# Kernel optimization log

Hardware: AMD Instinct MI355X
Metric: run time of the kernel (lower is better)

## Reference

```python
import jax, jax.numpy as jnp
import numpy as np

GAMMA = 0.99
ALPHA = 0.01
EPS = 1e-08


def discounted_returns(rewards, gamma):
    # reverse linear recurrence G_t = r_t + gamma * G_{t+1}, scanned over time (dim 0)
    def step(G, r):
        G = r + gamma * G
        return G, G
    G0 = jnp.zeros(rewards.shape[1:], dtype=rewards.dtype)
    _, returns = jax.lax.scan(step, G0, rewards, reverse=True)
    return returns


def setup_inputs() -> dict:
    key = jax.random.key(0)
    k1, k2, k3, k4, k5 = jax.random.split(key, 5)
    T, B = 8192, 4096
    return {
        "rewards": jax.random.normal(k1, (T, B), dtype=jnp.float32),
        "value_estimates": jax.random.normal(k2, (T, B), dtype=jnp.float32),
        "log_probs": jax.random.normal(k3, (T, B), dtype=jnp.float32),
        "entropies": jax.random.uniform(k4, (T, B), dtype=jnp.float32),
        "to_include": jax.random.randint(k5, (T, B), 0, 2) > 0,
    }


def reference(rewards, value_estimates, log_probs, entropies, to_include):
    returns = discounted_returns(rewards, GAMMA)

    mask = to_include.astype(returns.dtype)
    n = jnp.sum(mask)
    # first call: count=1 -> sg=0 -> running stats equal masked batch stats (detached)
    mean = jax.lax.stop_gradient(jnp.sum(returns * mask) / n)
    var = jnp.sum(jnp.square((returns - mean) * mask)) / (n - 1.0)  # torch .std() is unbiased
    std = jax.lax.stop_gradient(jnp.sqrt(var))

    returns = (returns - mean) / (std + EPS)
    advantages = returns - value_estimates

    critic_loss = jnp.sum(jnp.square(advantages) * mask)
    actor_terms = -log_probs * jax.lax.stop_gradient(advantages) - ALPHA * entropies
    actor_loss = jnp.sum(actor_terms * mask)
    return (critic_loss, actor_loss)
```

## Files before the change

kernel.cpp:

```cpp
#include <hip/hip_runtime.h>
#include <hip/hip_cooperative_groups.h>

namespace cg = cooperative_groups;


constexpr int T     = 8192;
constexpr int B     = 4096;
constexpr int B4    = B / 4;
constexpr int BLK   = 256;
constexpr int WAVES = BLK / 64;
constexpr int L     = 32;
constexpr int NC    = T / L;
constexpr int NTILE = NC * 4;
constexpr int GSZ   = 16;
constexpr int NGRP  = NC / GSZ;

constexpr float GAMMA_F = 0.99f;
constexpr double cpow(double g, int n) { double r = 1.0; for (int i = 0; i < n; ++i) r *= g; return r; }
constexpr float G32  = (float)cpow(0.99, L);
constexpr float G512 = (float)cpow(0.99, L * GSZ);

#define COMP(MJ, GX, RX, VX, LX, ZX)                 \
    do {                                             \
        GX = fmaf(GAMMA_F, GX, RX);                  \
        float mm = (MJ);                             \
        float Gm = mm * GX, vm = mm * VX, lm = mm * LX; \
        a[0] += mm; a[1] += Gm;                      \
        a[2] = fmaf(Gm, GX, a[2]);                   \
        a[3] = fmaf(Gm, VX, a[3]);                   \
        a[4] += vm; a[5] = fmaf(vm, VX, a[5]);       \
        a[6] = fmaf(lm, GX, a[6]); a[7] += lm;       \
        a[8] = fmaf(mm, ZX, a[8]);                   \
        a[9] = fmaf(lm, VX, a[9]);                   \
    } while (0)

#define MASK_I32 { int4 q = ((const int4*)mp)[e]; \
    m0 = q.x ? 1.f : 0.f; m1 = q.y ? 1.f : 0.f; m2 = q.z ? 1.f : 0.f; m3 = q.w ? 1.f : 0.f; }
#define MASK_U8  { uchar4 q = ((const uchar4*)mp)[e]; \
    m0 = q.x ? 1.f : 0.f; m1 = q.y ? 1.f : 0.f; m2 = q.z ? 1.f : 0.f; m3 = q.w ? 1.f : 0.f; }

#define ITER_BODY(MASKLOAD)                          \
    _Pragma("unroll 4")                              \
    for (int i = L - 1; i >= 0; --i) {               \
        int e = base + i * B4;                       \
        float4 r = rw[e], v = vv[e], l = lq[e], z = en[e]; \
        float m0, m1, m2, m3;                        \
        MASKLOAD;                                    \
        COMP(m0, G.x, r.x, v.x, l.x, z.x);           \
        COMP(m1, G.y, r.y, v.y, l.y, z.y);           \
        COMP(m2, G.z, r.z, v.z, l.z, z.z);           \
        COMP(m3, G.w, r.w, v.w, l.w, z.w);           \
    }

__device__ __forceinline__ float4 chunk_scan(const float4* __restrict__ rw, int base) {
    const float g2 = GAMMA_F * GAMMA_F;
    float4 e4 = make_float4(0.f, 0.f, 0.f, 0.f);
    float4 o4 = make_float4(0.f, 0.f, 0.f, 0.f);
    #pragma unroll
    for (int j = L / 2 - 1; j >= 0; --j) {
        float4 ro = rw[base + (2 * j + 1) * B4];
        float4 re = rw[base + (2 * j) * B4];
        o4.x = fmaf(g2, o4.x, ro.x); o4.y = fmaf(g2, o4.y, ro.y);
        o4.z = fmaf(g2, o4.z, ro.z); o4.w = fmaf(g2, o4.w, ro.w);
        e4.x = fmaf(g2, e4.x, re.x); e4.y = fmaf(g2, e4.y, re.y);
        e4.z = fmaf(g2, e4.z, re.z); e4.w = fmaf(g2, e4.w, re.w);
    }
    float4 s;
    s.x = fmaf(GAMMA_F, o4.x, e4.x); s.y = fmaf(GAMMA_F, o4.y, e4.y);
    s.z = fmaf(GAMMA_F, o4.z, e4.z); s.w = fmaf(GAMMA_F, o4.w, e4.w);
    return s;
}

__device__ __forceinline__ float4 chunk_carry(const float4* __restrict__ S,
                                              const float4* __restrict__ Hg,
                                              int c, int b) {
    const int g = c >> 4;
    const int gend = (g << 4) | (GSZ - 1);
    float4 X = make_float4(0.f, 0.f, 0.f, 0.f);
    float w = 1.f;
    for (int cc = c + 1; cc <= gend; ++cc) {
        float4 sv = S[(size_t)cc * B4 + b];
        X.x = fmaf(w, sv.x, X.x); X.y = fmaf(w, sv.y, X.y);
        X.z = fmaf(w, sv.z, X.z); X.w = fmaf(w, sv.w, X.w);
        w *= G32;
    }
    float4 hg = Hg[(size_t)g * B4 + b];
    X.x = fmaf(w, hg.x, X.x); X.y = fmaf(w, hg.y, X.y);
    X.z = fmaf(w, hg.z, X.z); X.w = fmaf(w, hg.w, X.w);
    return X;
}

__device__ __forceinline__ void fold_groups(const float4* __restrict__ S,
                                            float4* __restrict__ Sg,
                                            int idx) {
    int g = idx >> 10;
    int bb = idx & 1023;
    float4 X = make_float4(0.f, 0.f, 0.f, 0.f);
    float w = 1.f;
    #pragma unroll
    for (int j = 0; j < GSZ; ++j) {
        float4 sv = S[(size_t)(g * GSZ + j) * B4 + bb];
        X.x = fmaf(w, sv.x, X.x); X.y = fmaf(w, sv.y, X.y);
        X.z = fmaf(w, sv.z, X.z); X.w = fmaf(w, sv.w, X.w);
        w *= G32;
    }
    Sg[(size_t)g * B4 + bb] = X;
}

__device__ __forceinline__ void gscan_col(const float4* __restrict__ Sg,
                                          float4* __restrict__ Hg, int bb) {
    float4 h = make_float4(0.f, 0.f, 0.f, 0.f);
    #pragma unroll
    for (int g = NGRP - 1; g >= 0; --g) {
        Hg[(size_t)g * B4 + bb] = h;
        float4 sv = Sg[(size_t)g * B4 + bb];
        h.x = fmaf(G512, h.x, sv.x); h.y = fmaf(G512, h.y, sv.y);
        h.z = fmaf(G512, h.z, sv.z); h.w = fmaf(G512, h.w, sv.w);
    }
}

__device__ __forceinline__ void finalize(const double s[10], float* out) {
    double n = s[0], SG = s[1], SG2 = s[2], SGv = s[3], Sv = s[4];
    double Sv2 = s[5], SlpG = s[6], Slp = s[7], Sent = s[8], Slpv = s[9];
    double mean = SG / n;
    double css  = SG2 - 2.0 * mean * SG + mean * mean * n;
    double var  = css / (n - 1.0);
    double sd   = sqrt(var);
    double sc   = 1.0 / (sd + 1e-8);
    double critic = sc * sc * css - 2.0 * sc * (SGv - mean * Sv) + Sv2;
    double actor  = -sc * (SlpG - mean * Slp) + Slpv - 0.01 * Sent;
    out[0] = (float)critic;
    out[1] = (float)actor;
}

__device__ __forceinline__ void reduce10_store(double d[10], double* dst,
                                               double shd[WAVES][10], int tid) {
    #pragma unroll
    for (int k = 0; k < 10; ++k)
        #pragma unroll
        for (int off = 32; off; off >>= 1)
            d[k] += __shfl_down(d[k], off);
    int lane = tid & 63, wv = tid >> 6;
    if (lane == 0) {
        #pragma unroll
        for (int k = 0; k < 10; ++k) shd[wv][k] = d[k];
    }
    __syncthreads();
    if (tid == 0) {
        #pragma unroll
        for (int k = 0; k < 10; ++k) {
            double t = shd[0][k];
            #pragma unroll
            for (int ww = 1; ww < WAVES; ++ww) t += shd[ww][k];
            dst[k] = t;
        }
    }
}

__device__ __forceinline__ void final_reduce(const double* __restrict__ p1,
                                             double shd[WAVES][10],
                                             int tid, float* out) {
    double d[10];
    #pragma unroll
    for (int k = 0; k < 10; ++k) d[k] = 0.0;
    for (int i = tid; i < NTILE; i += BLK) {
        #pragma unroll
        for (int k = 0; k < 10; ++k) d[k] += p1[(size_t)i * 10 + k];
    }
    #pragma unroll
    for (int k = 0; k < 10; ++k)
        #pragma unroll
        for (int off = 32; off; off >>= 1)
            d[k] += __shfl_down(d[k], off);
    int lane = tid & 63, wv = tid >> 6;
    if (lane == 0) {
        #pragma unroll
        for (int k = 0; k < 10; ++k) shd[wv][k] = d[k];
    }
    __syncthreads();
    if (tid == 0) {
        double s[10];
        #pragma unroll
        for (int k = 0; k < 10; ++k) {
            double t = shd[0][k];
            #pragma unroll
            for (int ww = 1; ww < WAVES; ++ww) t += shd[ww][k];
            s[k] = t;
        }
        finalize(s, out);
    }
}

__global__ void __launch_bounds__(BLK, 4) k_all(
    const float4* __restrict__ rw, const float4* __restrict__ vv,
    const float4* __restrict__ lq, const float4* __restrict__ en,
    const void*  __restrict__ mp,
    float4* __restrict__ S, float4* __restrict__ Sg, float4* __restrict__ Hg,
    double* __restrict__ p1, float* __restrict__ out)
{
    cg::grid_group grid = cg::this_grid();
    const int tid = threadIdx.x;
    const int bid = blockIdx.x;
    const int c = bid >> 2, s = bid & 3;
    const int b = s * 256 + tid;
    const int base = c * L * B4 + b;

    __shared__ double shd[WAVES][10];
    __shared__ unsigned shp[WAVES];

    unsigned pv = 0;
    {
        const uint4* mq = (const uint4*)mp;
        #pragma unroll
        for (int it = 0; it < 4; ++it) {
            uint4 q = mq[it * BLK + tid];
            pv |= (q.x | q.y | q.z | q.w) & 0xFFFFFF00u;
        }
        #pragma unroll
        for (int off = 32; off; off >>= 1) pv |= __shfl_down(pv, off);
        if ((tid & 63) == 0) shp[tid >> 6] = pv;
        __syncthreads();
        pv = shp[0] | shp[1] | shp[2] | shp[3];
    }
    const bool is32 = (pv == 0);

    S[(size_t)c * B4 + b] = chunk_scan(rw, base);
    grid.sync();

    if (bid < NGRP * B4 / BLK) fold_groups(S, Sg, bid * BLK + tid);
    grid.sync();

    if (bid < B4 / BLK) gscan_col(Sg, Hg, bid * BLK + tid);
    grid.sync();

    {
        float4 G = chunk_carry(S, Hg, c, b);
        float a[10] = {0.f, 0.f, 0.f, 0.f, 0.f, 0.f, 0.f, 0.f, 0.f, 0.f};
        if (is32) { ITER_BODY(MASK_I32); }
        else      { ITER_BODY(MASK_U8); }
        double d[10];
        #pragma unroll
        for (int k = 0; k < 10; ++k) d[k] = (double)a[k];
        reduce10_store(d, p1 + (size_t)bid * 10, shd, tid);
    }
    grid.sync();

    if (bid == 0) final_reduce(p1, shd, tid, out);
}

__global__ void __launch_bounds__(BLK) k_scanf(const float4* __restrict__ rw,
                                               const void* __restrict__ mp,
                                               float4* __restrict__ S,
                                               int* __restrict__ dflag) {
    __shared__ unsigned shp[WAVES];
    const int tid = threadIdx.x, bid = blockIdx.x;
    const int c = bid >> 2, s = bid & 3;
    const int b = s * 256 + tid;
    S[(size_t)c * B4 + b] = chunk_scan(rw, c * L * B4 + b);
    if (bid == NTILE - 1) {
        unsigned pv = 0;
        const uint4* mq = (const uint4*)mp;
        #pragma unroll
        for (int it = 0; it < 4; ++it) {
            uint4 q = mq[it * BLK + tid];
            pv |= (q.x | q.y | q.z | q.w) & 0xFFFFFF00u;
        }
        #pragma unroll
        for (int off = 32; off; off >>= 1) pv |= __shfl_down(pv, off);
        if ((tid & 63) == 0) shp[tid >> 6] = pv;
        __syncthreads();
        if (tid == 0) *dflag = ((shp[0] | shp[1] | shp[2] | shp[3]) == 0) ? 1 : 0;
    }
}

__global__ void __launch_bounds__(BLK) k_foldf(const float4* __restrict__ S,
                                               float4* __restrict__ Sg) {
    fold_groups(S, Sg, blockIdx.x * BLK + threadIdx.x);
}

__global__ void __launch_bounds__(BLK) k_gscanf(const float4* __restrict__ Sg,
                                                float4* __restrict__ Hg) {
    gscan_col(Sg, Hg, blockIdx.x * BLK + threadIdx.x);
}

__global__ void __launch_bounds__(BLK) k_mainf(const float4* __restrict__ rw,
                                               const float4* __restrict__ vv,
                                               const float4* __restrict__ lq,
                                               const float4* __restrict__ en,
                                               const void*  __restrict__ mp,
                                               const int*   __restrict__ dflag,
                                               const float4* __restrict__ S,
                                               const float4* __restrict__ Hg,
                                               double* __restrict__ p1) {
    __shared__ double shd[WAVES][10];
    const int tid = threadIdx.x, bid = blockIdx.x;
    const int c = bid >> 2, s = bid & 3;
    const int b = s * 256 + tid;
    const int base = c * L * B4 + b;
    float4 G = chunk_carry(S, Hg, c, b);
    float a[10] = {0.f, 0.f, 0.f, 0.f, 0.f, 0.f, 0.f, 0.f, 0.f, 0.f};
    if (*dflag) { ITER_BODY(MASK_I32); }
    else        { ITER_BODY(MASK_U8); }
    double d[10];
    #pragma unroll
    for (int k = 0; k < 10; ++k) d[k] = (double)a[k];
    reduce10_store(d, p1 + (size_t)bid * 10, shd, tid);
}

__global__ void __launch_bounds__(BLK) k_finalf(const double* __restrict__ p1,
                                                float* __restrict__ out) {
    __shared__ double shd[WAVES][10];
    final_reduce(p1, shd, threadIdx.x, out);
}

extern "C" void kernel_launch(void* const* d_in, const int* in_sizes, int n_in,
                              void* d_out, int out_size, void* d_ws, size_t ws_size,
                              hipStream_t stream) {
    const float4* rw = (const float4*)d_in[0];
    const float4* vv = (const float4*)d_in[1];
    const float4* lq = (const float4*)d_in[2];
    const float4* en = (const float4*)d_in[3];
    const void*   mp = d_in[4];

    char* ws = (char*)d_ws;
    size_t off = 0;
    float4* S   = (float4*)(ws + off); off += (size_t)NC * B4 * 16;
    float4* Sg  = (float4*)(ws + off); off += (size_t)NGRP * B4 * 16;
    float4* Hg  = (float4*)(ws + off); off += (size_t)NGRP * B4 * 16;
    double* p1  = (double*)(ws + off); off += (size_t)NTILE * 10 * 8;
    int*  dflag = (int*)  (ws + off);
    float* outp = (float*)d_out;

    int dev = 0;
    (void)hipGetDevice(&dev);
    int coop = 0, ncu = 0, maxb = 0;
    (void)hipDeviceGetAttribute(&coop, hipDeviceAttributeCooperativeLaunch, dev);
    (void)hipDeviceGetAttribute(&ncu, hipDeviceAttributeMultiprocessorCount, dev);
    bool use_coop = false;
    if (coop) {
        if (hipOccupancyMaxActiveBlocksPerMultiprocessor(&maxb, k_all, BLK, 0)
                == hipSuccess && (long)maxb * ncu >= NTILE)
            use_coop = true;
    }
    if (use_coop) {
        void* args[] = { (void*)&rw, (void*)&vv, (void*)&lq, (void*)&en,
                         (void*)&mp, (void*)&S, (void*)&Sg, (void*)&Hg,
                         (void*)&p1, (void*)&outp };
        if (hipLaunchCooperativeKernel((void*)k_all, dim3(NTILE), dim3(BLK),
                                       args, 0, stream) != hipSuccess)
            use_coop = false;
    }
    if (!use_coop) {
        k_scanf <<<NTILE, BLK, 0, stream>>>(rw, mp, S, dflag);
        k_foldf <<<NGRP * B4 / BLK, BLK, 0, stream>>>(S, Sg);
        k_gscanf<<<B4 / BLK, BLK, 0, stream>>>(Sg, Hg);
        k_mainf <<<NTILE, BLK, 0, stream>>>(rw, vv, lq, en, mp, dflag, S, Hg, p1);
        k_finalf<<<1, BLK, 0, stream>>>(p1, outp);
    }
}
```

Before: 152.0 us.

## Single-pass input read with carry-correction coefficients instead of second sweep

```diff
diff --git a/kernel.cpp b/kernel.cpp
--- a/kernel.cpp
+++ b/kernel.cpp
@@ -14,11 +14,48 @@
 constexpr int NTILE = NC * 4;
 constexpr int GSZ   = 16;
 constexpr int NGRP  = NC / GSZ;
+constexpr int NTHR  = NTILE * BLK;
 
 constexpr float GAMMA_F = 0.99f;
 constexpr double cpow(double g, int n) { double r = 1.0; for (int i = 0; i < n; ++i) r *= g; return r; }
 constexpr float G32  = (float)cpow(0.99, L);
 constexpr float G512 = (float)cpow(0.99, L * GSZ);
+
+#define COMPC(MJ, GX, RX, VX, LX, ZX, C0X, C1X, C2X, C3X, C4X)   \
+    do {                                                         \
+        GX = fmaf(GAMMA_F, GX, RX);                              \
+        float mm = (MJ);                                         \
+        float Gm = mm * GX, vm = mm * VX, lm = mm * LX, mw = mm * w; \
+        a[0] += mm; a[1] += Gm;                                  \
+        a[2] = fmaf(Gm, GX, a[2]); a[3] = fmaf(Gm, VX, a[3]);    \
+        a[4] += vm; a[5] = fmaf(vm, VX, a[5]);                   \
+        a[6] = fmaf(lm, GX, a[6]); a[7] += lm;                   \
+        a[8] = fmaf(mm, ZX, a[8]); a[9] = fmaf(lm, VX, a[9]);    \
+        C0X += mw;                                               \
+        C1X = fmaf(mw, GX, C1X);                                 \
+        C2X = fmaf(mw, w,  C2X);                                 \
+        C3X = fmaf(mw, VX, C3X);                                 \
+        C4X = fmaf(mw, LX, C4X);                                 \
+    } while (0)
+
+#define MASK_I32 { int4 q = ((const int4*)mp)[e]; \
+    m0 = q.x ? 1.f : 0.f; m1 = q.y ? 1.f : 0.f; m2 = q.z ? 1.f : 0.f; m3 = q.w ? 1.f : 0.f; }
+#define MASK_U8  { uchar4 q = ((const uchar4*)mp)[e]; \
+    m0 = q.x ? 1.f : 0.f; m1 = q.y ? 1.f : 0.f; m2 = q.z ? 1.f : 0.f; m3 = q.w ? 1.f : 0.f; }
+
+#define ITER_BODYC(MASKLOAD)                         \
+    _Pragma("unroll 4")                              \
+    for (int i = L - 1; i >= 0; --i) {               \
+        int e = base + i * B4;                       \
+        float4 r = rw[e], v = vv[e], l = lq[e], z = en[e]; \
+        float m0, m1, m2, m3;                        \
+        MASKLOAD;                                    \
+        COMPC(m0, G.x, r.x, v.x, l.x, z.x, c0.x, c1.x, c2.x, c3.x, c4.x); \
+        COMPC(m1, G.y, r.y, v.y, l.y, z.y, c0.y, c1.y, c2.y, c3.y, c4.y); \
+        COMPC(m2, G.z, r.z, v.z, l.z, z.z, c0.z, c1.z, c2.z, c3.z, c4.z); \
+        COMPC(m3, G.w, r.w, v.w, l.w, z.w, c0.w, c1.w, c2.w, c3.w, c4.w); \
+        w *= GAMMA_F;                                \
+    }
 
 #define COMP(MJ, GX, RX, VX, LX, ZX)                 \
     do {                                             \
@@ -34,11 +71,6 @@
         a[9] = fmaf(lm, VX, a[9]);                   \
     } while (0)
 
-#define MASK_I32 { int4 q = ((const int4*)mp)[e]; \
-    m0 = q.x ? 1.f : 0.f; m1 = q.y ? 1.f : 0.f; m2 = q.z ? 1.f : 0.f; m3 = q.w ? 1.f : 0.f; }
-#define MASK_U8  { uchar4 q = ((const uchar4*)mp)[e]; \
-    m0 = q.x ? 1.f : 0.f; m1 = q.y ? 1.f : 0.f; m2 = q.z ? 1.f : 0.f; m3 = q.w ? 1.f : 0.f; }
-
 #define ITER_BODY(MASKLOAD)                          \
     _Pragma("unroll 4")                              \
     for (int i = L - 1; i >= 0; --i) {               \
@@ -91,8 +123,7 @@
 }
 
 __device__ __forceinline__ void fold_groups(const float4* __restrict__ S,
-                                            float4* __restrict__ Sg,
-                                            int idx) {
+                                            float4* __restrict__ Sg, int idx) {
     int g = idx >> 10;
     int bb = idx & 1023;
     float4 X = make_float4(0.f, 0.f, 0.f, 0.f);
@@ -157,37 +188,27 @@
     }
 }
 
-__device__ __forceinline__ void final_reduce(const double* __restrict__ p1,
-                                             double shd[WAVES][10],
-                                             int tid, float* out) {
-    double d[10];
-    #pragma unroll
-    for (int k = 0; k < 10; ++k) d[k] = 0.0;
-    for (int i = tid; i < NTILE; i += BLK) {
-        #pragma unroll
-        for (int k = 0; k < 10; ++k) d[k] += p1[(size_t)i * 10 + k];
-    }
-    #pragma unroll
-    for (int k = 0; k < 10; ++k)
+__device__ __forceinline__ void reduce4_store(double d[4], double* dst,
+                                              double shd[WAVES][10], int tid) {
+    #pragma unroll
+    for (int k = 0; k < 4; ++k)
         #pragma unroll
         for (int off = 32; off; off >>= 1)
             d[k] += __shfl_down(d[k], off);
     int lane = tid & 63, wv = tid >> 6;
     if (lane == 0) {
         #pragma unroll
-        for (int k = 0; k < 10; ++k) shd[wv][k] = d[k];
+        for (int k = 0; k < 4; ++k) shd[wv][k] = d[k];
     }
     __syncthreads();
     if (tid == 0) {
-        double s[10];
-        #pragma unroll
-        for (int k = 0; k < 10; ++k) {
+        #pragma unroll
+        for (int k = 0; k < 4; ++k) {
             double t = shd[0][k];
             #pragma unroll
             for (int ww = 1; ww < WAVES; ++ww) t += shd[ww][k];
-            s[k] = t;
-        }
-        finalize(s, out);
+            dst[k] = t;
+        }
     }
 }
 
@@ -196,7 +217,9 @@
     const float4* __restrict__ lq, const float4* __restrict__ en,
     const void*  __restrict__ mp,
     float4* __restrict__ S, float4* __restrict__ Sg, float4* __restrict__ Hg,
-    double* __restrict__ p1, float* __restrict__ out)
+    float4* __restrict__ CF0, float4* __restrict__ CF1, float4* __restrict__ CF2,
+    float4* __restrict__ CF3, float4* __restrict__ CF4,
+    double* __restrict__ p1, double* __restrict__ p2, float* __restrict__ out)
 {
     cg::grid_group grid = cg::this_grid();
     const int tid = threadIdx.x;
@@ -204,6 +227,7 @@
     const int c = bid >> 2, s = bid & 3;
     const int b = s * 256 + tid;
     const int base = c * L * B4 + b;
+    const size_t gt = (size_t)bid * BLK + tid;
 
     __shared__ double shd[WAVES][10];
     __shared__ unsigned shp[WAVES];
@@ -224,7 +248,22 @@
     }
     const bool is32 = (pv == 0);
 
-    S[(size_t)c * B4 + b] = chunk_scan(rw, base);
+    {
+        float4 G  = make_float4(0.f, 0.f, 0.f, 0.f);
+        float4 c0 = G, c1 = G, c2 = G, c3 = G, c4 = G;
+        float a[10] = {0.f, 0.f, 0.f, 0.f, 0.f, 0.f, 0.f, 0.f, 0.f, 0.f};
+        float w = GAMMA_F;
+        if (is32) { ITER_BODYC(MASK_I32); }
+        else      { ITER_BODYC(MASK_U8); }
+
+        S[(size_t)c * B4 + b] = G;
+        CF0[gt] = c0; CF1[gt] = c1; CF2[gt] = c2; CF3[gt] = c3; CF4[gt] = c4;
+
+        double d[10];
+        #pragma unroll
+        for (int k = 0; k < 10; ++k) d[k] = (double)a[k];
+        reduce10_store(d, p1 + (size_t)bid * 10, shd, tid);
+    }
     grid.sync();
 
     if (bid < NGRP * B4 / BLK) fold_groups(S, Sg, bid * BLK + tid);
@@ -234,18 +273,54 @@
     grid.sync();
 
     {
-        float4 G = chunk_carry(S, Hg, c, b);
-        float a[10] = {0.f, 0.f, 0.f, 0.f, 0.f, 0.f, 0.f, 0.f, 0.f, 0.f};
-        if (is32) { ITER_BODY(MASK_I32); }
-        else      { ITER_BODY(MASK_U8); }
+        float4 X = chunk_carry(S, Hg, c, b);
+        float4 c0 = CF0[gt], c1 = CF1[gt], c2 = CF2[gt], c3 = CF3[gt], c4 = CF4[gt];
+        double hx = X.x, hy = X.y, hz = X.z, hw = X.w;
+        double d[4];
+        d[0] = hx * c0.x + hy * c0.y + hz * c0.z + hw * c0.w;
+        d[1] = 2.0 * (hx * c1.x + hy * c1.y + hz * c1.z + hw * c1.w)
+             + (hx * hx * c2.x + hy * hy * c2.y + hz * hz * c2.z + hw * hw * c2.w);
+        d[2] = hx * c3.x + hy * c3.y + hz * c3.z + hw * c3.w;
+        d[3] = hx * c4.x + hy * c4.y + hz * c4.z + hw * c4.w;
+        reduce4_store(d, p2 + (size_t)bid * 4, shd, tid);
+    }
+    grid.sync();
+
+    if (bid == 0) {
         double d[10];
         #pragma unroll
-        for (int k = 0; k < 10; ++k) d[k] = (double)a[k];
-        reduce10_store(d, p1 + (size_t)bid * 10, shd, tid);
-    }
-    grid.sync();
-
-    if (bid == 0) final_reduce(p1, shd, tid, out);
+        for (int k = 0; k < 10; ++k) d[k] = 0.0;
+        for (int i = tid; i < NTILE; i += BLK) {
+            #pragma unroll
+            for (int k = 0; k < 10; ++k) d[k] += p1[(size_t)i * 10 + k];
+            d[1] += p2[(size_t)i * 4 + 0];
+            d[2] += p2[(size_t)i * 4 + 1];
+            d[3] += p2[(size_t)i * 4 + 2];
+            d[6] += p2[(size_t)i * 4 + 3];
+        }
+        #pragma unroll
+        for (int k = 0; k < 10; ++k)
+            #pragma unroll
+            for (int off = 32; off; off >>= 1)
+                d[k] += __shfl_down(d[k], off);
+        int lane = tid & 63, wv = tid >> 6;
+        if (lane == 0) {
+            #pragma unroll
+            for (int k = 0; k < 10; ++k) shd[wv][k] = d[k];
+        }
+        __syncthreads();
+        if (tid == 0) {
+            double sum[10];
+            #pragma unroll
+            for (int k = 0; k < 10; ++k) {
+                double t = shd[0][k];
+                #pragma unroll
+                for (int ww = 1; ww < WAVES; ++ww) t += shd[ww][k];
+                sum[k] = t;
+            }
+            finalize(sum, out);
+        }
+    }
 }
 
 __global__ void __launch_bounds__(BLK) k_scanf(const float4* __restrict__ rw,
@@ -310,7 +385,36 @@
 __global__ void __launch_bounds__(BLK) k_finalf(const double* __restrict__ p1,
                                                 float* __restrict__ out) {
     __shared__ double shd[WAVES][10];
-    final_reduce(p1, shd, threadIdx.x, out);
+    const int tid = threadIdx.x;
+    double d[10];
+    #pragma unroll
+    for (int k = 0; k < 10; ++k) d[k] = 0.0;
+    for (int i = tid; i < NTILE; i += BLK) {
+        #pragma unroll
+        for (int k = 0; k < 10; ++k) d[k] += p1[(size_t)i * 10 + k];
+    }
+    #pragma unroll
+    for (int k = 0; k < 10; ++k)
+        #pragma unroll
+        for (int off = 32; off; off >>= 1)
+            d[k] += __shfl_down(d[k], off);
+    int lane = tid & 63, wv = tid >> 6;
+    if (lane == 0) {
+        #pragma unroll
+        for (int k = 0; k < 10; ++k) shd[wv][k] = d[k];
+    }
+    __syncthreads();
+    if (tid == 0) {
+        double s[10];
+        #pragma unroll
+        for (int k = 0; k < 10; ++k) {
+            double t = shd[0][k];
+            #pragma unroll
+            for (int ww = 1; ww < WAVES; ++ww) t += shd[ww][k];
+            s[k] = t;
+        }
+        finalize(s, out);
+    }
 }
 
 extern "C" void kernel_launch(void* const* d_in, const int* in_sizes, int n_in,
@@ -327,7 +431,13 @@
     float4* S   = (float4*)(ws + off); off += (size_t)NC * B4 * 16;
     float4* Sg  = (float4*)(ws + off); off += (size_t)NGRP * B4 * 16;
     float4* Hg  = (float4*)(ws + off); off += (size_t)NGRP * B4 * 16;
+    float4* CF0 = (float4*)(ws + off); off += (size_t)NTHR * 16;
+    float4* CF1 = (float4*)(ws + off); off += (size_t)NTHR * 16;
+    float4* CF2 = (float4*)(ws + off); off += (size_t)NTHR * 16;
+    float4* CF3 = (float4*)(ws + off); off += (size_t)NTHR * 16;
+    float4* CF4 = (float4*)(ws + off); off += (size_t)NTHR * 16;
     double* p1  = (double*)(ws + off); off += (size_t)NTILE * 10 * 8;
+    double* p2  = (double*)(ws + off); off += (size_t)NTILE * 4 * 8;
     int*  dflag = (int*)  (ws + off);
     float* outp = (float*)d_out;
 
@@ -345,7 +455,8 @@
     if (use_coop) {
         void* args[] = { (void*)&rw, (void*)&vv, (void*)&lq, (void*)&en,
                          (void*)&mp, (void*)&S, (void*)&Sg, (void*)&Hg,
-                         (void*)&p1, (void*)&outp };
+                         (void*)&CF0, (void*)&CF1, (void*)&CF2, (void*)&CF3,
+                         (void*)&CF4, (void*)&p1, (void*)&p2, (void*)&outp };
         if (hipLaunchCooperativeKernel((void*)k_all, dim3(NTILE), dim3(BLK),
                                        args, 0, stream) != hipSuccess)
             use_coop = false;
```

New measurement: 150.3 us. No clear change (-1.1%).
